# Optimization experiments

Hardware: AMD Instinct MI355X
Metric: run time of the kernel (lower is better)

Reference implementation:

```python
import jax, jax.numpy as jnp
import numpy as np


def setup_inputs() -> dict:
    key = jax.random.key(0)
    k1, k2, k3 = jax.random.split(key, 3)
    B, C, H, W = 4, 16, 64, 64
    F, K = 32, 3
    x = jax.random.normal(k1, (B, C, H, W), dtype=jnp.float32)
    # Pade coefficients per (out_channel, in_channel, a, b): numerator deg 5, denom deg 4.
    nums = jax.random.normal(k2, (F, C, K, K, 6), dtype=jnp.float32) * 0.3
    denoms = jax.random.normal(k3, (F, C, K, K, 4), dtype=jnp.float32) * 0.3
    return {"x": x, "nums": nums, "denoms": denoms}


def _rational_conv(x, nums, denoms):
    B, C, H, W = x.shape
    F, _, K, _, _ = nums.shape
    p = (K - 1) // 2
    # pad spatially, move channels last: (B, H+2p, W+2p, C)
    xp = jnp.pad(x, ((0, 0), (0, 0), (p, p), (p, p))).transpose(0, 2, 3, 1)
    # im2col patches: stack the K*K shifted views -> (B, H, W, K2, C)
    patches = jnp.stack(
        [xp[:, a:a + H, b:b + W, :] for a in range(K) for b in range(K)], axis=3
    )
    # powers x^0..x^5 built by repeated multiply (safe for negative bases)
    pws = [jnp.ones_like(patches)]
    for _ in range(5):
        pws.append(pws[-1] * patches)
    pw = jnp.stack(pws, axis=-1)                         # (B,H,W,K2,C,6)
    nums_r = nums.reshape(F, C, K * K, 6)                # (a,b) flattened a*K+b, matches patch order
    denoms_r = denoms.reshape(F, C, K * K, 4)
    # P(x) = sum_n a_n x^n ; Q(x) = 1 + |sum_m b_m x^m|, m=1..4  (Pade version A)
    P = jnp.einsum('bhwkcn,fckn->bhwfkc', pw, nums_r)
    Q = 1.0 + jnp.abs(jnp.einsum('bhwkcm,fckm->bhwfkc', pw[..., 1:5], denoms_r))
    out = (P / Q).sum(axis=(4, 5))                       # (B,H,W,F)
    return out.transpose(0, 3, 1, 2)                     # (B,F,H,W)


def reference(x, nums, denoms):
    return _rational_conv(x, nums, denoms)
```

## Files before the change

kernel.cpp:

```cpp
#include <hip/hip_runtime.h>
#include <hip/hip_fp16.h>

#define B_ 4
#define C_ 16
#define H_ 64
#define W_ 64
#define F_ 32
#define S_ 66
#define CHW_ (S_ * S_)
#define XN_ (B_ * 8 * CHW_)
#define CPAIR 90
#define NC_ (F_ * 8 * 9)

typedef _Float16 hvec2 __attribute__((ext_vector_type(2)));

__global__ __launch_bounds__(256)
void pack_kernel(const float* __restrict__ x,
                 const float* __restrict__ nums, const float* __restrict__ denoms,
                 __half2* __restrict__ xw, __half2* __restrict__ cw) {
    const int i = blockIdx.x * 256 + threadIdx.x;
    if (i < XN_) {
        const int cc = i % S_;
        int t = i / S_;
        const int r  = t % S_;
        t /= S_;
        const int pr = t % 8;
        const int b  = t / 8;
        float lo = 0.f, hi = 0.f;
        if (r >= 1 && r <= H_ && cc >= 1 && cc <= W_) {
            const int sp = (r - 1) * W_ + (cc - 1);
            lo = x[((size_t)(b * C_ + pr)     ) * (H_ * W_) + sp];
            hi = x[((size_t)(b * C_ + pr + 8)) * (H_ * W_) + sp];
        }
        xw[i] = __halves2half2(__float2half_rn(lo), __float2half_rn(hi));
    } else if (i < XN_ + NC_) {
        const int k = i - XN_;
        const int tap = k % 9;
        const int pr  = (k / 9) % 8;
        const int f   = k / 72;
        __half2* o = cw + ((size_t)(f * 8 + pr) * 9 + tap) * 10;
        const size_t nlo = (((size_t)f * C_ + pr)     * 9 + tap) * 6;
        const size_t nhi = (((size_t)f * C_ + pr + 8) * 9 + tap) * 6;
        for (int q = 0; q < 6; ++q)
            o[q] = __halves2half2(__float2half_rn(nums[nlo + q]), __float2half_rn(nums[nhi + q]));
        const size_t dlo = (((size_t)f * C_ + pr)     * 9 + tap) * 4;
        const size_t dhi = (((size_t)f * C_ + pr + 8) * 9 + tap) * 4;
        for (int q = 0; q < 4; ++q)
            o[6 + q] = __halves2half2(__float2half_rn(denoms[dlo + q]), __float2half_rn(denoms[dhi + q]));
    }
}

__global__ __launch_bounds__(512)
void ka_rconv_kernel(const __half2* __restrict__ xw,
                     const __half2* __restrict__ cw,
                     float* __restrict__ out) {
    __shared__ float red[8 * 4 * 64];

    const int tid = threadIdx.x;
    const int col = tid & 63;
    const int wg  = tid >> 6;

    int bid = blockIdx.x;
    const int f  = bid & 31;  bid >>= 5;
    const int t4 = bid & 15;  bid >>= 4;
    const int b  = bid;
    const int gy0 = t4 * 4;

    const int pr = __builtin_amdgcn_readfirstlane(wg);
    const __half2* ce = cw + (size_t)(f * 8 + pr) * CPAIR;
    const __half2* xbase = xw + ((size_t)(b * 8 + pr) * S_ + gy0) * S_ + col;

    const __half2 one = __halves2half2(__half(1.0f), __half(1.0f));
    float acc[4] = {0.f, 0.f, 0.f, 0.f};

    uint3 rv[6];
    #pragma unroll
    for (int k = 0; k < 6; ++k)
        rv[k] = *(const uint3*)(xbase + k * S_);

    #pragma unroll
    for (int t = 0; t < 9; ++t) {
        const __half2 n0 = ce[t*10+0], n1 = ce[t*10+1], n2 = ce[t*10+2];
        const __half2 n3 = ce[t*10+3], n4 = ce[t*10+4], n5 = ce[t*10+5];
        const __half2 d0 = ce[t*10+6], d1 = ce[t*10+7];
        const __half2 d2 = ce[t*10+8], d3 = ce[t*10+9];
        const int a = t / 3, j = t % 3;
        #pragma unroll
        for (int p = 0; p < 4; ++p) {
            const uint3 r3 = rv[p + a];
            const unsigned u = (j == 0) ? r3.x : (j == 1) ? r3.y : r3.z;
            const __half2 xp = __builtin_bit_cast(__half2, u);

            __half2 P = __hfma2(n5, xp, n4);
            P = __hfma2(P, xp, n3);
            P = __hfma2(P, xp, n2);
            P = __hfma2(P, xp, n1);
            P = __hfma2(P, xp, n0);

            __half2 Sd = __hfma2(d3, xp, d2);
            Sd = __hfma2(Sd, xp, d1);
            Sd = __hfma2(Sd, xp, d0);
            Sd = __hmul2(Sd, xp);

            const __half2 Q = __hadd2(one, __habs2(Sd));
            const __half2 R = h2rcp(Q);
            acc[p] = __builtin_amdgcn_fdot2(__builtin_bit_cast(hvec2, P),
                                            __builtin_bit_cast(hvec2, R),
                                            acc[p], false);
        }
    }

    #pragma unroll
    for (int p = 0; p < 4; ++p)
        red[(wg * 4 + p) * 64 + col] = acc[p];
    __syncthreads();
    if (wg < 4) {
        float s = 0.f;
        #pragma unroll
        for (int q = 0; q < 8; ++q)
            s += red[(q * 4 + wg) * 64 + col];
        out[(((size_t)b * F_ + f) * H_ + gy0 + wg) * W_ + col] = s;
    }
}

extern "C" void kernel_launch(void* const* d_in, const int* in_sizes, int n_in,
                              void* d_out, int out_size, void* d_ws, size_t ws_size,
                              hipStream_t stream) {
    const float* x      = (const float*)d_in[0];
    const float* nums   = (const float*)d_in[1];
    const float* denoms = (const float*)d_in[2];
    float* outp = (float*)d_out;
    __half2* xw = (__half2*)d_ws;
    __half2* cwp = xw + XN_;

    pack_kernel<<<(XN_ + NC_ + 255) / 256, 256, 0, stream>>>(x, nums, denoms, xw, cwp);
    dim3 grid(B_ * 16 * F_);
    ka_rconv_kernel<<<grid, 512, 0, stream>>>(xw, cwp, outp);
}
```

Measured before the change: 78.36 us.

## Fuse packing into the rational conv kernel using shuffles and LDS coefficients

```diff
diff --git a/kernel.cpp b/kernel.cpp
--- a/kernel.cpp
+++ b/kernel.cpp
@@ -6,54 +6,23 @@
 #define H_ 64
 #define W_ 64
 #define F_ 32
-#define S_ 66
-#define CHW_ (S_ * S_)
-#define XN_ (B_ * 8 * CHW_)
-#define CPAIR 90
-#define NC_ (F_ * 8 * 9)
 
 typedef _Float16 hvec2 __attribute__((ext_vector_type(2)));
 
-__global__ __launch_bounds__(256)
-void pack_kernel(const float* __restrict__ x,
-                 const float* __restrict__ nums, const float* __restrict__ denoms,
-                 __half2* __restrict__ xw, __half2* __restrict__ cw) {
-    const int i = blockIdx.x * 256 + threadIdx.x;
-    if (i < XN_) {
-        const int cc = i % S_;
-        int t = i / S_;
-        const int r  = t % S_;
-        t /= S_;
-        const int pr = t % 8;
-        const int b  = t / 8;
-        float lo = 0.f, hi = 0.f;
-        if (r >= 1 && r <= H_ && cc >= 1 && cc <= W_) {
-            const int sp = (r - 1) * W_ + (cc - 1);
-            lo = x[((size_t)(b * C_ + pr)     ) * (H_ * W_) + sp];
-            hi = x[((size_t)(b * C_ + pr + 8)) * (H_ * W_) + sp];
-        }
-        xw[i] = __halves2half2(__float2half_rn(lo), __float2half_rn(hi));
-    } else if (i < XN_ + NC_) {
-        const int k = i - XN_;
-        const int tap = k % 9;
-        const int pr  = (k / 9) % 8;
-        const int f   = k / 72;
-        __half2* o = cw + ((size_t)(f * 8 + pr) * 9 + tap) * 10;
-        const size_t nlo = (((size_t)f * C_ + pr)     * 9 + tap) * 6;
-        const size_t nhi = (((size_t)f * C_ + pr + 8) * 9 + tap) * 6;
-        for (int q = 0; q < 6; ++q)
-            o[q] = __halves2half2(__float2half_rn(nums[nlo + q]), __float2half_rn(nums[nhi + q]));
-        const size_t dlo = (((size_t)f * C_ + pr)     * 9 + tap) * 4;
-        const size_t dhi = (((size_t)f * C_ + pr + 8) * 9 + tap) * 4;
-        for (int q = 0; q < 4; ++q)
-            o[6 + q] = __halves2half2(__float2half_rn(denoms[dlo + q]), __float2half_rn(denoms[dhi + q]));
-    }
+static __device__ __forceinline__ __half2 pk2(float lo, float hi) {
+    auto v = __builtin_amdgcn_cvt_pkrtz(lo, hi);
+    return __builtin_bit_cast(__half2, v);
+}
+static __device__ __forceinline__ __half2 bc2(unsigned u) {
+    return __builtin_bit_cast(__half2, u);
 }
 
 __global__ __launch_bounds__(512)
-void ka_rconv_kernel(const __half2* __restrict__ xw,
-                     const __half2* __restrict__ cw,
+void ka_fused_kernel(const float* __restrict__ x,
+                     const float* __restrict__ nums,
+                     const float* __restrict__ denoms,
                      float* __restrict__ out) {
+    __shared__ __half2 cLds[8 * 9 * 12];
     __shared__ float red[8 * 4 * 64];
 
     const int tid = threadIdx.x;
@@ -62,34 +31,79 @@
 
     int bid = blockIdx.x;
     const int f  = bid & 31;  bid >>= 5;
-    const int t4 = bid & 15;  bid >>= 4;
-    const int b  = bid;
+    const int t4 = bid & 15;
+    const int b  = bid >> 4;
     const int gy0 = t4 * 4;
 
     const int pr = __builtin_amdgcn_readfirstlane(wg);
-    const __half2* ce = cw + (size_t)(f * 8 + pr) * CPAIR;
-    const __half2* xbase = xw + ((size_t)(b * 8 + pr) * S_ + gy0) * S_ + col;
+
+    const float* xlo = x + ((size_t)(b * C_ + pr))     * (H_ * W_) + col;
+    const float* xhi = x + ((size_t)(b * C_ + pr + 8)) * (H_ * W_) + col;
+    float vlo[6], vhi[6];
+    #pragma unroll
+    for (int k = 0; k < 6; ++k) {
+        const int r = gy0 + k - 1;
+        vlo[k] = 0.f; vhi[k] = 0.f;
+        if ((unsigned)r < (unsigned)H_) {
+            vlo[k] = xlo[r * W_];
+            vhi[k] = xhi[r * W_];
+        }
+    }
+
+    {
+        const int base_lo = (f * C_ + pr) * 9;
+        const int base_hi = (f * C_ + pr + 8) * 9;
+        #pragma unroll
+        for (int e0 = 0; e0 < 128; e0 += 64) {
+            const int e = col + e0;
+            if (e < 90) {
+                const int tap = e / 10;
+                const int q   = e - tap * 10;
+                float a, c;
+                if (q < 6) {
+                    a = nums[(size_t)(base_lo + tap) * 6 + q];
+                    c = nums[(size_t)(base_hi + tap) * 6 + q];
+                } else {
+                    a = denoms[(size_t)(base_lo + tap) * 4 + (q - 6)];
+                    c = denoms[(size_t)(base_hi + tap) * 4 + (q - 6)];
+                }
+                cLds[(wg * 9 + tap) * 12 + q] = pk2(a, c);
+            }
+        }
+    }
+
+    uint3 rv[6];
+    #pragma unroll
+    for (int k = 0; k < 6; ++k) {
+        const unsigned u0 = __builtin_bit_cast(unsigned, pk2(vlo[k], vhi[k]));
+        unsigned um = (unsigned)__shfl_up((int)u0, 1);
+        unsigned up = (unsigned)__shfl_down((int)u0, 1);
+        if (col == 0)  um = 0u;
+        if (col == 63) up = 0u;
+        rv[k].x = um; rv[k].y = u0; rv[k].z = up;
+    }
+
+    __syncthreads();
 
     const __half2 one = __halves2half2(__half(1.0f), __half(1.0f));
     float acc[4] = {0.f, 0.f, 0.f, 0.f};
-
-    uint3 rv[6];
-    #pragma unroll
-    for (int k = 0; k < 6; ++k)
-        rv[k] = *(const uint3*)(xbase + k * S_);
+    const __half2* cb = &cLds[wg * 9 * 12];
 
     #pragma unroll
     for (int t = 0; t < 9; ++t) {
-        const __half2 n0 = ce[t*10+0], n1 = ce[t*10+1], n2 = ce[t*10+2];
-        const __half2 n3 = ce[t*10+3], n4 = ce[t*10+4], n5 = ce[t*10+5];
-        const __half2 d0 = ce[t*10+6], d1 = ce[t*10+7];
-        const __half2 d2 = ce[t*10+8], d3 = ce[t*10+9];
+        const uint4 wA = *(const uint4*)(cb + t * 12);
+        const uint4 wB = *(const uint4*)(cb + t * 12 + 4);
+        const uint2 wC = *(const uint2*)(cb + t * 12 + 8);
+        const __half2 n0 = bc2(wA.x), n1 = bc2(wA.y), n2 = bc2(wA.z), n3 = bc2(wA.w);
+        const __half2 n4 = bc2(wB.x), n5 = bc2(wB.y);
+        const __half2 d0 = bc2(wB.z), d1 = bc2(wB.w);
+        const __half2 d2 = bc2(wC.x), d3 = bc2(wC.y);
         const int a = t / 3, j = t % 3;
         #pragma unroll
         for (int p = 0; p < 4; ++p) {
             const uint3 r3 = rv[p + a];
             const unsigned u = (j == 0) ? r3.x : (j == 1) ? r3.y : r3.z;
-            const __half2 xp = __builtin_bit_cast(__half2, u);
+            const __half2 xp = bc2(u);
 
             __half2 P = __hfma2(n5, xp, n4);
             P = __hfma2(P, xp, n3);
@@ -129,11 +143,6 @@
     const float* x      = (const float*)d_in[0];
     const float* nums   = (const float*)d_in[1];
     const float* denoms = (const float*)d_in[2];
-    float* outp = (float*)d_out;
-    __half2* xw = (__half2*)d_ws;
-    __half2* cwp = xw + XN_;
-
-    pack_kernel<<<(XN_ + NC_ + 255) / 256, 256, 0, stream>>>(x, nums, denoms, xw, cwp);
-    dim3 grid(B_ * 16 * F_);
-    ka_rconv_kernel<<<grid, 512, 0, stream>>>(xw, cwp, outp);
+    (void)d_ws; (void)ws_size;
+    ka_fused_kernel<<<dim3(B_ * 16 * F_), 512, 0, stream>>>(x, nums, denoms, (float*)d_out);
 }
```

New measurement: 78.39 us. No clear change (+0.0%).
